# Kernel optimization log

Measured on AMD Instinct MI355X. Metric: run time of the kernel, lower is better.

The kernel has to match this reference:

```python
import jax, jax.numpy as jnp
import numpy as np

C = 64; NET = 32; K = 3; G = 4; GC = C // G; P = K * K
STRIDE = 1; PAD = 1; DIL = 1; OFFSET_SCALE = 1.0
BN_EPS = 1e-5; LN_EPS = 1e-6


def conv2d(x, w, b, groups=1, pad=1):
    # x: (N,C,H,W), w: (O, I//groups, kh, kw)
    y = jax.lax.conv_general_dilated(
        x, w, (1, 1), [(pad, pad), (pad, pad)],
        feature_group_count=groups,
        dimension_numbers=('NCHW', 'OIHW', 'NCHW'))
    return y + b[None, :, None, None]


def dcnv3_core(x, offset, mask):
    """Faithful port of dcnv3_core_pytorch (InternImage).
    x: (N,H,W,C) channels-last; offset: (N,H,W,G*P*2); mask: (N,H,W,G*P) (softmaxed).
    grid_sample(bilinear, zeros padding, align_corners=False) done manually."""
    xp = jnp.pad(x, ((0, 0), (PAD, PAD), (PAD, PAD), (0, 0)))
    N, Hin, Win, _ = xp.shape
    Ho, Wo = offset.shape[1], offset.shape[2]
    # reference points in normalized [0,1] coords (x first, y second)
    start = (DIL * (K - 1)) // 2 + 0.5
    ref_x = (start + jnp.arange(Wo, dtype=jnp.float32) * STRIDE) / Win  # (Wo,)
    ref_y = (start + jnp.arange(Ho, dtype=jnp.float32) * STRIDE) / Hin  # (Ho,)
    ref = jnp.stack(jnp.broadcast_arrays(ref_x[None, :], ref_y[:, None]), axis=-1)  # (Ho,Wo,2)
    # dilation grid (kernel tap offsets, torch meshgrid 'ij' flatten order: w-major)
    kv = (jnp.arange(K, dtype=jnp.float32) * DIL - (DIL * (K - 1)) // 2)
    gx, gy = jnp.meshgrid(kv / Win, kv / Hin, indexing='ij')
    grid = jnp.stack([gx, gy], -1).reshape(P, 2)  # (P,2), same for every group
    # sampling locations, normalized: (N,Ho,Wo,G,P,2)
    off = offset.reshape(N, Ho, Wo, G, P, 2) * (OFFSET_SCALE / jnp.array([Win, Hin], jnp.float32))
    loc = ref[None, :, :, None, None, :] + grid[None, None, None, None, :, :] * OFFSET_SCALE + off
    # grid_sample align_corners=False: pixel = loc*size - 0.5  (since g = 2*loc-1)
    px = loc[..., 0] * Win - 0.5
    py = loc[..., 1] * Hin - 0.5
    x0 = jnp.floor(px); y0 = jnp.floor(py)
    ix0 = x0.astype(jnp.int32); iy0 = y0.astype(jnp.int32)
    wx1 = px - x0; wy1 = py - y0; wx0 = 1.0 - wx1; wy0 = 1.0 - wy1
    xg = xp.reshape(N, Hin, Win, G, GC)
    n_idx = jnp.arange(N)[:, None, None, None, None]
    g_idx = jnp.arange(G)[None, None, None, :, None]

    def sample(ix, iy):
        valid = ((ix >= 0) & (ix < Win) & (iy >= 0) & (iy < Hin)).astype(xg.dtype)
        v = xg[n_idx, jnp.clip(iy, 0, Hin - 1), jnp.clip(ix, 0, Win - 1), g_idx]  # (N,Ho,Wo,G,P,GC)
        return v * valid[..., None]

    val = (sample(ix0, iy0) * (wx0 * wy0)[..., None]
           + sample(ix0 + 1, iy0) * (wx1 * wy0)[..., None]
           + sample(ix0, iy0 + 1) * (wx0 * wy1)[..., None]
           + sample(ix0 + 1, iy0 + 1) * (wx1 * wy1)[..., None])
    out = jnp.einsum('nhwgpc,nhwgp->nhwgc', val, mask.reshape(N, Ho, Wo, G, P))
    return out.reshape(N, Ho, Wo, C)


def setup_inputs() -> dict:
    key = jax.random.key(0)
    ks = jax.random.split(key, 16)
    N, H, W = 4, 128, 128
    f = lambda k, shp, s=1.0: jax.random.normal(k, shp, jnp.float32) * s
    return {
        'input_x': f(ks[0], (N, C, H, W)),
        'input_y': f(ks[1], (N, NET, H, W)),
        'enc_w': f(ks[2], (NET, C), 0.05), 'enc_b': jnp.zeros((NET,), jnp.float32),
        'bn_g': jnp.ones((NET,), jnp.float32), 'bn_b': jnp.zeros((NET,), jnp.float32),
        'bn_m': jnp.zeros((NET,), jnp.float32), 'bn_v': jnp.ones((NET,), jnp.float32),
        'gru_wz': f(ks[3], (NET, 2 * NET, 3, 3), 0.05), 'gru_bz': jnp.zeros((NET,), jnp.float32),
        'gru_wr': f(ks[4], (NET, 2 * NET, 3, 3), 0.05), 'gru_br': jnp.zeros((NET,), jnp.float32),
        'gru_wq': f(ks[5], (NET, 2 * NET, 3, 3), 0.05), 'gru_bq': jnp.zeros((NET,), jnp.float32),
        'dw_w': f(ks[6], (C, 1, 3, 3), 0.1), 'dw_b': jnp.zeros((C,), jnp.float32),
        'ln_g': jnp.ones((C,), jnp.float32), 'ln_b': jnp.zeros((C,), jnp.float32),
        'off_w': f(ks[7], (G * P * 2, C), 0.1), 'off_b': f(ks[8], (G * P * 2,), 0.1),
        'mask_w': f(ks[9], (G * P, C), 0.1), 'mask_b': jnp.zeros((G * P,), jnp.float32),
        'inp_w': f(ks[10], (C, C), 0.1), 'inp_b': jnp.zeros((C,), jnp.float32),
        'out_w': f(ks[11], (C, C), 0.1), 'out_b': jnp.zeros((C,), jnp.float32),
    }


def reference(input_x, input_y, enc_w, enc_b, bn_g, bn_b, bn_m, bn_v,
              gru_wz, gru_bz, gru_wr, gru_br, gru_wq, gru_bq,
              dw_w, dw_b, ln_g, ln_b, off_w, off_b, mask_w, mask_b,
              inp_w, inp_b, out_w, out_b):
    N, _, H, W = input_x.shape
    # encoder: 1x1 Conv + BN(eval) + SiLU
    e = jnp.einsum('nchw,oc->nohw', input_x, enc_w) + enc_b[None, :, None, None]
    e = (e - bn_m[None, :, None, None]) * jax.lax.rsqrt(bn_v + BN_EPS)[None, :, None, None]
    e = e * bn_g[None, :, None, None] + bn_b[None, :, None, None]
    x_en = jax.nn.silu(e)
    # ConvGRU: h' = (1-z)*h + z*q
    hx = jnp.concatenate([input_y, x_en], axis=1)
    z = jax.nn.sigmoid(conv2d(hx, gru_wz, gru_bz))
    r = jax.nn.sigmoid(conv2d(hx, gru_wr, gru_br))
    q = jnp.tanh(conv2d(jnp.concatenate([r * input_y, x_en], axis=1), gru_wq, gru_bq))
    h = (1.0 - z) * input_y + z * q  # (N,NET,H,W)
    # channels-last main path
    inp = input_x.transpose(0, 2, 3, 1)  # (N,H,W,C)
    x = inp @ inp_w.T + inp_b
    # depthwise conv on gru state -> LN (channels_last) -> GELU
    y = conv2d(h, dw_w, dw_b, groups=NET).transpose(0, 2, 3, 1)  # (N,H,W,C)
    mu = y.mean(-1, keepdims=True)
    var = ((y - mu) ** 2).mean(-1, keepdims=True)
    y = (y - mu) * jax.lax.rsqrt(var + LN_EPS) * ln_g + ln_b
    y = jax.nn.gelu(y, approximate=False)
    offset = y @ off_w.T + off_b  # (N,H,W,G*P*2)
    m = y @ mask_w.T + mask_b
    m = jax.nn.softmax(m.reshape(N, H, W, G, P), axis=-1).reshape(N, H, W, G * P)
    x = dcnv3_core(x, offset, m)
    x = x @ out_w.T + out_b
    return jax.nn.silu(x.transpose(0, 3, 1, 2)), h
```

## Files before the change

kernel.cpp:

```cpp
#include <hip/hip_runtime.h>
#include <hip/hip_bf16.h>

typedef __hip_bfloat16 bf16;
typedef short short8v __attribute__((ext_vector_type(8)));
typedef short short4v __attribute__((ext_vector_type(4)));
typedef float float4v __attribute__((ext_vector_type(4)));

static __device__ __forceinline__ float b2f(bf16 v){ return __bfloat162float(v); }
static __device__ __forceinline__ bf16 f2b(float v){ return __float2bfloat16(v); }
static __device__ __forceinline__ float bu2f(unsigned short u){ return __uint_as_float(((unsigned)u) << 16); }
static __device__ __forceinline__ short f2bs(float v){ bf16 t = __float2bfloat16(v); return *(short*)&t; }

#define WT 128
#define HWT 16384

#define OFF_ENC   0
#define OFF_ENCSC 2048
#define OFF_ENCSH 2080
#define OFF_BZ    20544
#define OFF_BR    39008
#define OFF_BQ    57472
#define OFF_DWP   57504
#define OFF_DWB   58080
#define OFF_LNG   58144
#define OFF_LNB   58208
#define OFF_OMB   65184
#define OFF_WINP  65296
#define OFF_BINP  69392
#define OFF_BOUT  73552
#define NW_TOTAL  73616
#define NBF_ZR    36864
#define NBF_Q     18432
#define NBF_OM    7168
#define NBF_OUT   4096
#define NPREP     (NW_TOTAL + NBF_ZR + NBF_Q + NBF_OM + NBF_OUT)
#define NHALO     2064
#define NTOT      (NPREP + NHALO)

#define B_WZRB  294912
#define B_WQB   368640
#define B_WOMB  405504
#define B_WOUTB 419840
#define B_HXP   428544
#define B_QINP  9081344
#define B_ZBUF  17734144
#define B_XL    428544

__global__ void k_prep(
    const float* __restrict__ enc_w, const float* __restrict__ enc_b,
    const float* __restrict__ bn_g, const float* __restrict__ bn_b,
    const float* __restrict__ bn_m, const float* __restrict__ bn_v,
    const float* __restrict__ gwz, const float* __restrict__ gbz,
    const float* __restrict__ gwr, const float* __restrict__ gbr,
    const float* __restrict__ gwq, const float* __restrict__ gbq,
    const float* __restrict__ dww, const float* __restrict__ dwb,
    const float* __restrict__ lng, const float* __restrict__ lnb,
    const float* __restrict__ offw, const float* __restrict__ offb,
    const float* __restrict__ maskw, const float* __restrict__ maskb,
    const float* __restrict__ inpw, const float* __restrict__ inpb,
    const float* __restrict__ outw, const float* __restrict__ outb,
    float* __restrict__ Wp, bf16* __restrict__ wzrb, bf16* __restrict__ wqb,
    bf16* __restrict__ womb, bf16* __restrict__ woutb,
    bf16* __restrict__ hxp, bf16* __restrict__ qinp) {
  int i = blockIdx.x * blockDim.x + threadIdx.x;
  if (i >= NTOT) return;
  if (i >= NPREP) {
    int t = i - NPREP;
    int img = t / 516, r = t % 516;
    int ph, pw;
    if (r < 130) { ph = 0; pw = r; }
    else if (r < 260) { ph = 129; pw = r - 130; }
    else if (r < 388) { ph = r - 260 + 1; pw = 0; }
    else { ph = r - 388 + 1; pw = 129; }
    size_t pb = (((size_t)img * 130 + ph) * 130 + pw) * 64;
    uint4 zz = make_uint4(0, 0, 0, 0);
    #pragma unroll
    for (int k = 0; k < 8; ++k) {
      ((uint4*)(hxp + pb))[k] = zz;
      ((uint4*)(qinp + pb))[k] = zz;
    }
    return;
  }
  if (i >= NW_TOTAL) {
    int d = i - NW_TOTAL;
    if (d < NBF_ZR) {
      int t = d / 9216, rem = d % 9216;
      int kc = rem / 512, rem2 = rem % 512;
      int ln = rem2 >> 3, j = rem2 & 7;
      int n = t * 16 + (ln & 15);
      int cin = (kc & 1) * 32 + ((ln >> 4) << 3) + j;
      int tap = kc >> 1;
      float v = (n < 32) ? gwz[(n*64 + cin)*9 + tap] : gwr[((n-32)*64 + cin)*9 + tap];
      wzrb[d] = f2b(v);
    } else if (d < NBF_ZR + NBF_Q) {
      int d2 = d - NBF_ZR;
      int t = d2 / 9216, rem = d2 % 9216;
      int kc = rem / 512, rem2 = rem % 512;
      int ln = rem2 >> 3, j = rem2 & 7;
      int n = t * 16 + (ln & 15);
      int cin = (kc & 1) * 32 + ((ln >> 4) << 3) + j;
      int tap = kc >> 1;
      wqb[d2] = f2b(gwq[(n*64 + cin)*9 + tap]);
    } else if (d < NBF_ZR + NBF_Q + NBF_OM) {
      int d3 = d - NBF_ZR - NBF_Q;
      int wv = d3 / 1024, rem = d3 % 1024;
      int kc = rem / 512, rem2 = rem % 512;
      int ln = rem2 >> 3, j = rem2 & 7;
      int jcol = wv * 16 + (ln & 15);
      int c = kc * 32 + ((ln >> 4) << 3) + j;
      float v = (jcol < 72) ? offw[jcol*64 + c] : ((jcol < 108) ? maskw[(jcol-72)*64 + c] : 0.f);
      womb[d3] = f2b(v);
    } else {
      int d4 = d - NBF_ZR - NBF_Q - NBF_OM;
      int wv = d4 / 1024, rem = d4 % 1024;
      int kc = rem / 512, rem2 = rem % 512;
      int ln = rem2 >> 3, j = rem2 & 7;
      int o = wv * 16 + (ln & 15);
      int c = kc * 32 + ((ln >> 4) << 3) + j;
      woutb[d4] = f2b(outw[o*64 + c]);
    }
    return;
  }
  float v;
  if (i < 2048) { int c = i >> 5, o = i & 31; v = enc_w[o*64 + c]; }
  else if (i < 2080) { int o = i - 2048; v = bn_g[o] * rsqrtf(bn_v[o] + 1e-5f); }
  else if (i < 2112) { int o = i - 2080;
    float sc = bn_g[o] * rsqrtf(bn_v[o] + 1e-5f);
    v = (enc_b[o] - bn_m[o]) * sc + bn_b[o]; }
  else if (i < 20544) { v = 0.f; }
  else if (i < 20576) { v = gbz[i - OFF_BZ]; }
  else if (i < 39008) { v = 0.f; }
  else if (i < 39040) { v = gbr[i - OFF_BR]; }
  else if (i < 57472) { v = 0.f; }
  else if (i < 57504) { v = gbq[i - OFF_BQ]; }
  else if (i < 58080) { int d = i - OFF_DWP; int tap = d >> 6, o = d & 63; v = dww[o*9 + tap]; }
  else if (i < 58144) { v = dwb[i - OFF_DWB]; }
  else if (i < 58208) { v = lng[i - OFF_LNG]; }
  else if (i < 58272) { v = lnb[i - OFF_LNB]; }
  else if (i < 65184) { v = 0.f; }
  else if (i < 65292) { int j = i - OFF_OMB; v = (j < 72) ? offb[j] : maskb[j-72]; }
  else if (i < 65296) { v = 0.f; }
  else if (i < 69392) { int d = i - OFF_WINP; int c = d >> 6, o = d & 63; v = inpw[o*64 + c]; }
  else if (i < 69456) { v = inpb[i - OFF_BINP]; }
  else if (i < 73552) { v = 0.f; }
  else { v = outb[i - OFF_BOUT]; }
  Wp[i] = v;
}

__global__ void __launch_bounds__(256) k_pre(
    const float* __restrict__ X, const float* __restrict__ Y,
    const float* __restrict__ Wp, bf16* __restrict__ hxp, bf16* __restrict__ qinp) {
  __shared__ float xls[4096];
  int tid = threadIdx.x;
  int px = tid & 63, sect = tid >> 6;
  int img = blockIdx.z, h = blockIdx.y, w0 = blockIdx.x * 64;
  int hw = h * WT + w0 + px;
  const float* xp = X + (size_t)img * (64 * HWT) + hw;
  #pragma unroll
  for (int i = 0; i < 16; ++i) {
    int c = sect * 16 + i;
    xls[c * 64 + px] = xp[c * HWT];
  }
  const float* yp = Y + (size_t)img * (32 * HWT) + hw;
  bf16 yv[8];
  #pragma unroll
  for (int i = 0; i < 8; ++i) yv[i] = f2b(yp[(sect * 8 + i) * HWT]);
  size_t pb = (((size_t)img * 130 + h + 1) * 130 + (w0 + px + 1)) * 64;
  *(uint4*)(hxp + pb + sect * 8) = *(const uint4*)yv;
  __syncthreads();
  float aen[8];
  #pragma unroll
  for (int o = 0; o < 8; ++o) aen[o] = 0.f;
  for (int k = 0; k < 64; ++k) {
    float a = xls[k * 64 + px];
    const float* we = Wp + OFF_ENC + k * 32 + sect * 8;
    #pragma unroll
    for (int o = 0; o < 8; ++o) aen[o] += a * we[o];
  }
  bf16 xe[8];
  #pragma unroll
  for (int o = 0; o < 8; ++o) {
    int oo = sect * 8 + o;
    float e = aen[o] * Wp[OFF_ENCSC + oo] + Wp[OFF_ENCSH + oo];
    xe[o] = f2b(e / (1.f + __expf(-e)));
  }
  *(uint4*)(hxp + pb + 32 + sect * 8) = *(const uint4*)xe;
  *(uint4*)(qinp + pb + 32 + sect * 8) = *(const uint4*)xe;
}

__global__ void __launch_bounds__(256) k_zr(
    const float* __restrict__ Wp,
    const bf16* __restrict__ hxp, const bf16* __restrict__ wzrb,
    bf16* __restrict__ qinp, bf16* __restrict__ zbuf) {
  __shared__ short zt[32 * 132];
  __shared__ short ryt[128 * 40];
  int tid = threadIdx.x;
  int wv = tid >> 6, ln = tid & 63;
  int quad = ln >> 4, lm = ln & 15;
  int img = blockIdx.z, h = blockIdx.y;
  int p0 = wv * 32;
  const short* hs = (const short*)hxp;
  const short* ws = (const short*)wzrb;
  size_t rowb = ((size_t)img * 130 + h + 1) * 130;
  const short* ab0 = hs + (rowb + p0 + lm + 1) * 64 + quad * 8;
  const short* ab1 = ab0 + 16 * 64;
  short8v a0[18], a1[18];
  #pragma unroll
  for (int kc = 0; kc < 18; ++kc) {
    const int tap = kc >> 1, cin0 = (kc & 1) * 32;
    const int dd = (tap / 3 - 1) * 130 + (tap % 3 - 1);
    a0[kc] = *(const short8v*)(ab0 + dd * 64 + cin0);
    a1[kc] = *(const short8v*)(ab1 + dd * 64 + cin0);
  }
  float4v acc[8];
  #pragma unroll
  for (int t = 0; t < 8; ++t) acc[t] = (float4v){0.f, 0.f, 0.f, 0.f};
  #pragma unroll
  for (int kc = 0; kc < 18; ++kc) {
    #pragma unroll
    for (int t = 0; t < 4; ++t) {
      short8v b = *(const short8v*)(ws + ((t * 18 + kc) * 64 + ln) * 8);
      acc[t*2]   = __builtin_amdgcn_mfma_f32_16x16x32_bf16(a0[kc], b, acc[t*2], 0, 0, 0);
      acc[t*2+1] = __builtin_amdgcn_mfma_f32_16x16x32_bf16(a1[kc], b, acc[t*2+1], 0, 0, 0);
    }
  }
  #pragma unroll
  for (int mt = 0; mt < 2; ++mt) {
    #pragma unroll
    for (int t = 0; t < 2; ++t) {
      int n = t * 16 + lm;
      float bz = Wp[OFF_BZ + n];
      short zp[4];
      #pragma unroll
      for (int ri = 0; ri < 4; ++ri)
        zp[ri] = f2bs(1.f / (1.f + __expf(-(acc[t*2+mt][ri] + bz))));
      *(short4v*)(zt + n * 132 + p0 + mt * 16 + quad * 4) = *(const short4v*)zp;
    }
  }
  #pragma unroll
  for (int mt = 0; mt < 2; ++mt) {
    #pragma unroll
    for (int t = 2; t < 4; ++t) {
      int c = (t - 2) * 16 + lm;
      float br = Wp[OFF_BR + c];
      #pragma unroll
      for (int ri = 0; ri < 4; ++ri) {
        int px = p0 + mt * 16 + quad * 4 + ri;
        float rv = 1.f / (1.f + __expf(-(acc[t*2+mt][ri] + br)));
        float yy = b2f(hxp[(rowb + px + 1) * 64 + c]);
        ryt[px * 40 + c] = f2bs(rv * yy);
      }
    }
  }
  __syncthreads();
  {
    int n2 = tid >> 3, pq = tid & 7;
    short8v z0 = *(const short8v*)(zt + n2 * 132 + pq * 16);
    short8v z1 = *(const short8v*)(zt + n2 * 132 + pq * 16 + 8);
    short* zo = (short*)zbuf + (((size_t)img * 128 + h) * 32 + n2) * 128 + pq * 16;
    *(short8v*)zo = z0;
    *(short8v*)(zo + 8) = z1;
  }
  {
    int px = tid >> 1, chalf = tid & 1;
    short8v r0 = *(const short8v*)(ryt + px * 40 + chalf * 16);
    short8v r1 = *(const short8v*)(ryt + px * 40 + chalf * 16 + 8);
    short* qo = (short*)qinp + (rowb + px + 1) * 64 + chalf * 16;
    *(short8v*)qo = r0;
    *(short8v*)(qo + 8) = r1;
  }
}

__global__ void __launch_bounds__(256) k_qg(
    const float* __restrict__ Y, const float* __restrict__ Wp,
    const bf16* __restrict__ qinp, const bf16* __restrict__ wqb,
    const bf16* __restrict__ zbuf, float* __restrict__ outh) {
  __shared__ float hout[32 * 132];
  int tid = threadIdx.x;
  int wv = tid >> 6, ln = tid & 63;
  int quad = ln >> 4, lm = ln & 15;
  int img = blockIdx.z, h = blockIdx.y;
  int p0 = wv * 32;
  const short* qs = (const short*)qinp;
  const short* ws = (const short*)wqb;
  size_t rowb = ((size_t)img * 130 + h + 1) * 130;
  const short* ab0 = qs + (rowb + p0 + lm + 1) * 64 + quad * 8;
  const short* ab1 = ab0 + 16 * 64;
  short8v a0[18], a1[18];
  #pragma unroll
  for (int kc = 0; kc < 18; ++kc) {
    const int tap = kc >> 1, cin0 = (kc & 1) * 32;
    const int dd = (tap / 3 - 1) * 130 + (tap % 3 - 1);
    a0[kc] = *(const short8v*)(ab0 + dd * 64 + cin0);
    a1[kc] = *(const short8v*)(ab1 + dd * 64 + cin0);
  }
  float4v acc[4];
  #pragma unroll
  for (int t = 0; t < 4; ++t) acc[t] = (float4v){0.f, 0.f, 0.f, 0.f};
  #pragma unroll
  for (int kc = 0; kc < 18; ++kc) {
    #pragma unroll
    for (int t = 0; t < 2; ++t) {
      short8v b = *(const short8v*)(ws + ((t * 18 + kc) * 64 + ln) * 8);
      acc[t*2]   = __builtin_amdgcn_mfma_f32_16x16x32_bf16(a0[kc], b, acc[t*2], 0, 0, 0);
      acc[t*2+1] = __builtin_amdgcn_mfma_f32_16x16x32_bf16(a1[kc], b, acc[t*2+1], 0, 0, 0);
    }
  }
  #pragma unroll
  for (int mt = 0; mt < 2; ++mt) {
    #pragma unroll
    for (int t = 0; t < 2; ++t) {
      int n = t * 16 + lm;
      float bq = Wp[OFF_BQ + n];
      float4 hv;
      hv.x = acc[t*2+mt][0] + bq; hv.y = acc[t*2+mt][1] + bq;
      hv.z = acc[t*2+mt][2] + bq; hv.w = acc[t*2+mt][3] + bq;
      *(float4*)(hout + n * 132 + p0 + mt * 16 + quad * 4) = hv;
    }
  }
  __syncthreads();
  const short* zbb = (const short*)zbuf + ((size_t)img * 128 + h) * 32 * 128;
  #pragma unroll
  for (int r = 0; r < 4; ++r) {
    int n = (tid >> 5) + r * 8;
    int px4 = (tid & 31) * 4;
    float4 hv = *(const float4*)(hout + n * 132 + px4);
    uint2 zz = *(const uint2*)(zbb + n * 128 + px4);
    size_t gb = ((size_t)img * 32 + n) * HWT + h * 128 + px4;
    float4 yv = *(const float4*)(Y + gb);
    float z0 = bu2f((unsigned short)(zz.x & 0xFFFFu)), z1 = bu2f((unsigned short)(zz.x >> 16));
    float z2 = bu2f((unsigned short)(zz.y & 0xFFFFu)), z3 = bu2f((unsigned short)(zz.y >> 16));
    float4 o;
    o.x = (1.f - z0) * yv.x + z0 * tanhf(hv.x);
    o.y = (1.f - z1) * yv.y + z1 * tanhf(hv.y);
    o.z = (1.f - z2) * yv.z + z2 * tanhf(hv.z);
    o.w = (1.f - z3) * yv.w + z3 * tanhf(hv.w);
    *(float4*)(outh + gb) = o;
  }
}

__global__ void __launch_bounds__(256) k_xl(
    const float* __restrict__ X, const float* __restrict__ Wp, bf16* __restrict__ xl) {
  __shared__ float xls[4096];
  int tid = threadIdx.x;
  int px = tid & 63, sect = tid >> 6;
  int img = blockIdx.z, h = blockIdx.y, w0 = blockIdx.x * 64;
  int hw = h * WT + w0 + px;
  const float* xp = X + (size_t)img * (64 * HWT) + hw;
  #pragma unroll
  for (int i = 0; i < 16; ++i) {
    int c = sect * 16 + i;
    xls[c * 64 + px] = xp[c * HWT];
  }
  __syncthreads();
  float acc[16];
  #pragma unroll
  for (int o = 0; o < 16; ++o) acc[o] = Wp[OFF_BINP + sect * 16 + o];
  for (int k = 0; k < 64; ++k) {
    float a = xls[k * 64 + px];
    const float* wr = Wp + OFF_WINP + k * 64 + sect * 16;
    #pragma unroll
    for (int o = 0; o < 16; ++o) acc[o] += a * wr[o];
  }
  bf16 ov[16];
  #pragma unroll
  for (int o = 0; o < 16; ++o) ov[o] = f2b(acc[o]);
  bf16* op = xl + ((size_t)img * HWT + hw) * 64 + sect * 16;
  ((uint4*)op)[0] = ((const uint4*)ov)[0];
  ((uint4*)op)[1] = ((const uint4*)ov)[1];
}

#define LDS_PSA  0
#define LDS_PSB  2048
#define LDS_STAT 4096
#define LDS_Y    4608
#define LDS_OM   13824
#define LDS_TOT  28416

__global__ void __launch_bounds__(512) k_mega(
    const float* __restrict__ Wp, const float* __restrict__ hb,
    const bf16* __restrict__ xl, const bf16* __restrict__ womb,
    const bf16* __restrict__ woutb, float* __restrict__ out0) {
  __shared__ char smem[LDS_TOT];
  float* psa  = (float*)(smem + LDS_PSA);
  float* psb  = (float*)(smem + LDS_PSB);
  float* stat = (float*)(smem + LDS_STAT);
  short* yls  = (short*)(smem + LDS_Y);
  short* omls = (short*)(smem + LDS_OM);
  short* vls  = (short*)(smem + LDS_Y);

  int tid = threadIdx.x;
  int img = blockIdx.z, h = blockIdx.y, w0 = blockIdx.x * 64;

  int wloc = tid & 63, part = tid >> 6;
  int w = w0 + wloc;
  float yv[8];
  {
    const float* hn = hb + (size_t)img * (32 * HWT);
    #pragma unroll
    for (int i = 0; i < 8; ++i) yv[i] = Wp[OFF_DWB + part*8 + i];
    #pragma unroll
    for (int tap = 0; tap < 9; ++tap) {
      int dy = tap / 3 - 1, dx = tap % 3 - 1;
      int hh = h + dy, ww = w + dx;
      bool ok = ((unsigned)hh < 128u) && ((unsigned)ww < 128u);
      int off = hh * WT + ww;
      #pragma unroll
      for (int j = 0; j < 4; ++j) {
        int cin = part * 4 + j;
        float a = ok ? hn[cin * HWT + off] : 0.f;
        yv[2*j]   += a * Wp[OFF_DWP + tap*64 + part*8 + 2*j];
        yv[2*j+1] += a * Wp[OFF_DWP + tap*64 + part*8 + 2*j+1];
      }
    }
  }
  float lsum = 0.f, lsq = 0.f;
  #pragma unroll
  for (int i = 0; i < 8; ++i) { lsum += yv[i]; lsq += yv[i]*yv[i]; }
  psa[part * 64 + wloc] = lsum;
  psb[part * 64 + wloc] = lsq;
  __syncthreads();
  if (tid < 64) {
    float s = 0.f, q = 0.f;
    #pragma unroll
    for (int p = 0; p < 8; ++p) { s += psa[p*64 + tid]; q += psb[p*64 + tid]; }
    float mu = s * (1.f/64.f);
    float var = q * (1.f/64.f) - mu * mu;
    stat[tid*2] = mu;
    stat[tid*2+1] = rsqrtf(var + 1e-6f);
  }
  __syncthreads();
  {
    float mu = stat[wloc*2], inv = stat[wloc*2+1];
    bf16 tmp[8];
    #pragma unroll
    for (int i = 0; i < 8; ++i) {
      int c = part*8 + i;
      float v = (yv[i] - mu) * inv * Wp[OFF_LNG + c] + Wp[OFF_LNB + c];
      tmp[i] = f2b(0.5f * v * (1.f + erff(v * 0.70710678118654752f)));
    }
    *(short8v*)(yls + wloc*72 + part*8) = *(const short8v*)tmp;
  }
  __syncthreads();

  int wv = tid >> 6, ln = tid & 63, quad = ln >> 4, lm = ln & 15;
  if (wv < 7) {
    const short* wb = (const short*)womb;
    float4v acc[4];
    #pragma unroll
    for (int mt = 0; mt < 4; ++mt) acc[mt] = (float4v){0.f,0.f,0.f,0.f};
    #pragma unroll
    for (int kc = 0; kc < 2; ++kc) {
      short8v b = *(const short8v*)(wb + ((wv * 2 + kc) * 64 + ln) * 8);
      #pragma unroll
      for (int mt = 0; mt < 4; ++mt) {
        short8v a = *(const short8v*)(yls + (mt*16 + lm)*72 + kc*32 + quad*8);
        acc[mt] = __builtin_amdgcn_mfma_f32_16x16x32_bf16(a, b, acc[mt], 0, 0, 0);
      }
    }
    float bias = Wp[OFF_OMB + wv*16 + lm];
    #pragma unroll
    for (int mt = 0; mt < 4; ++mt) {
      #pragma unroll
      for (int ri = 0; ri < 4; ++ri)
        omls[(mt*16 + quad*4 + ri)*114 + wv*16 + lm] = f2bs(acc[mt][ri] + bias);
    }
  }
  __syncthreads();

  {
    int px = tid >> 3, g = (tid >> 1) & 3, half = tid & 1;
    const short* oml = omls + px*114;
    float m[9];
    #pragma unroll
    for (int p = 0; p < 9; ++p) m[p] = bu2f((unsigned short)oml[72 + g*9 + p]);
    float mx = m[0];
    #pragma unroll
    for (int p = 1; p < 9; ++p) mx = fmaxf(mx, m[p]);
    float sum = 0.f;
    #pragma unroll
    for (int p = 0; p < 9; ++p) { m[p] = __expf(m[p] - mx); sum += m[p]; }
    float rs = 1.f / sum;
    int wg = w0 + px;
    const bf16* xn = xl + (size_t)img * (HWT * 64);
    float acc[8];
    #pragma unroll
    for (int i = 0; i < 8; ++i) acc[i] = 0.f;
    for (int p = 0; p < 9; ++p) {
      float bx = (float)(wg + p / 3 - 1);
      float by = (float)(h + p % 3 - 1);
      float ox = bu2f((unsigned short)oml[g*18 + p*2]);
      float oy = bu2f((unsigned short)oml[g*18 + p*2 + 1]);
      float mk = m[p] * rs;
      float pxx = bx + ox, pyy = by + oy;
      float fx = floorf(pxx), fy = floorf(pyy);
      int jx0 = (int)fx, jy0 = (int)fy;
      float wx1 = pxx - fx, wy1 = pyy - fy;
      float wx0 = 1.f - wx1, wy0 = 1.f - wy1;
      int cjx[4] = { jx0, jx0 + 1, jx0, jx0 + 1 };
      int cjy[4] = { jy0, jy0, jy0 + 1, jy0 + 1 };
      float cw[4] = { wx0*wy0, wx1*wy0, wx0*wy1, wx1*wy1 };
      #pragma unroll
      for (int k = 0; k < 4; ++k) {
        if ((unsigned)cjx[k] < 128u && (unsigned)cjy[k] < 128u) {
          float cf = mk * cw[k];
          const bf16* s = xn + (size_t)(cjy[k] * WT + cjx[k]) * 64 + g * 16 + half * 8;
          uint4 u0 = *(const uint4*)(s);
          const unsigned uu[4] = {u0.x,u0.y,u0.z,u0.w};
          #pragma unroll
          for (int q = 0; q < 4; ++q) {
            acc[2*q]     += cf * bu2f((unsigned short)(uu[q] & 0xFFFFu));
            acc[2*q + 1] += cf * bu2f((unsigned short)(uu[q] >> 16));
          }
        }
      }
    }
    bf16 tmp[8];
    #pragma unroll
    for (int i = 0; i < 8; ++i) tmp[i] = f2b(acc[i]);
    *(short8v*)(vls + px*72 + g*16 + half*8) = *(const short8v*)tmp;
  }
  __syncthreads();

  if (wv < 4) {
    const short* wb = (const short*)woutb;
    float4v acc[4];
    #pragma unroll
    for (int mt = 0; mt < 4; ++mt) acc[mt] = (float4v){0.f,0.f,0.f,0.f};
    #pragma unroll
    for (int kc = 0; kc < 2; ++kc) {
      short8v b = *(const short8v*)(wb + ((wv * 2 + kc) * 64 + ln) * 8);
      #pragma unroll
      for (int mt = 0; mt < 4; ++mt) {
        short8v a = *(const short8v*)(vls + (mt*16 + lm)*72 + kc*32 + quad*8);
        acc[mt] = __builtin_amdgcn_mfma_f32_16x16x32_bf16(a, b, acc[mt], 0, 0, 0);
      }
    }
    int ch = wv*16 + lm;
    float bias = Wp[OFF_BOUT + ch];
    #pragma unroll
    for (int mt = 0; mt < 4; ++mt) {
      float4 v;
      float s0 = acc[mt][0] + bias; v.x = s0 / (1.f + __expf(-s0));
      float s1 = acc[mt][1] + bias; v.y = s1 / (1.f + __expf(-s1));
      float s2 = acc[mt][2] + bias; v.z = s2 / (1.f + __expf(-s2));
      float s3 = acc[mt][3] + bias; v.w = s3 / (1.f + __expf(-s3));
      *(float4*)(out0 + ((size_t)img*64 + ch)*HWT + h*128 + w0 + mt*16 + quad*4) = v;
    }
  }
}

extern "C" void kernel_launch(void* const* d_in, const int* in_sizes, int n_in,
                              void* d_out, int out_size, void* d_ws, size_t ws_size,
                              hipStream_t stream) {
  const float* input_x = (const float*)d_in[0];
  const float* input_y = (const float*)d_in[1];

  float* Wp = (float*)d_ws;
  bf16* WZRB  = (bf16*)((char*)d_ws + B_WZRB);
  bf16* WQB   = (bf16*)((char*)d_ws + B_WQB);
  bf16* WOMB  = (bf16*)((char*)d_ws + B_WOMB);
  bf16* WOUTB = (bf16*)((char*)d_ws + B_WOUTB);
  bf16* HXP   = (bf16*)((char*)d_ws + B_HXP);
  bf16* QINP  = (bf16*)((char*)d_ws + B_QINP);
  bf16* ZBUF  = (bf16*)((char*)d_ws + B_ZBUF);
  bf16* XL    = (bf16*)((char*)d_ws + B_XL);
  float* out0 = (float*)d_out;
  float* outh = (float*)d_out + 4194304;

  k_prep<<<dim3((NTOT + 255)/256), dim3(256), 0, stream>>>(
      (const float*)d_in[2], (const float*)d_in[3], (const float*)d_in[4], (const float*)d_in[5],
      (const float*)d_in[6], (const float*)d_in[7], (const float*)d_in[8], (const float*)d_in[9],
      (const float*)d_in[10], (const float*)d_in[11], (const float*)d_in[12], (const float*)d_in[13],
      (const float*)d_in[14], (const float*)d_in[15], (const float*)d_in[16], (const float*)d_in[17],
      (const float*)d_in[18], (const float*)d_in[19], (const float*)d_in[20], (const float*)d_in[21],
      (const float*)d_in[22], (const float*)d_in[23], (const float*)d_in[24], (const float*)d_in[25],
      Wp, WZRB, WQB, WOMB, WOUTB, HXP, QINP);
  k_pre<<<dim3(2, 128, 4), dim3(256), 0, stream>>>(input_x, input_y, Wp, HXP, QINP);
  k_zr <<<dim3(1, 128, 4), dim3(256), 0, stream>>>(Wp, HXP, WZRB, QINP, ZBUF);
  k_qg <<<dim3(1, 128, 4), dim3(256), 0, stream>>>(input_y, Wp, QINP, WQB, ZBUF, outh);
  k_xl <<<dim3(2, 128, 4), dim3(256), 0, stream>>>(input_x, Wp, XL);
  k_mega<<<dim3(2, 128, 4), dim3(512), 0, stream>>>(Wp, outh, XL, WOMB, WOUTB, out0);
}
```

Before: 257.4 us.

## Split GRU conv rows across two blocks and spread output projection over all waves

k_zr and k_qg now handle 64 output pixels per block instead of 128, with each wave computing one 16-pixel M-tile. This doubles their grids and drops the second A-fragment set, cutting register pressure, and launch_bounds now request 4 blocks per SM. In k_mega the final 1x1 output projection is spread across all 8 waves, two tiles each, instead of only 4 waves doing 4 tiles. The aim is more parallelism and occupancy. The cost is that each B weight fragment is now fetched by more waves, and each block does less work relative to its launch and sync overhead.

Result: no change. 259.8 us (+0.9%).

```diff
diff --git a/kernel.cpp b/kernel.cpp
--- a/kernel.cpp
+++ b/kernel.cpp
@@ -112,10 +112,10 @@
       womb[d3] = f2b(v);
     } else {
       int d4 = d - NBF_ZR - NBF_Q - NBF_OM;
-      int wv = d4 / 1024, rem = d4 % 1024;
+      int nt = d4 / 1024, rem = d4 % 1024;
       int kc = rem / 512, rem2 = rem % 512;
       int ln = rem2 >> 3, j = rem2 & 7;
-      int o = wv * 16 + (ln & 15);
+      int o = nt * 16 + (ln & 15);
       int c = kc * 32 + ((ln >> 4) << 3) + j;
       woutb[d4] = f2b(outw[o*64 + c]);
     }
@@ -188,145 +188,128 @@
   *(uint4*)(qinp + pb + 32 + sect * 8) = *(const uint4*)xe;
 }
 
-__global__ void __launch_bounds__(256) k_zr(
+__global__ void __launch_bounds__(256, 4) k_zr(
     const float* __restrict__ Wp,
     const bf16* __restrict__ hxp, const bf16* __restrict__ wzrb,
     bf16* __restrict__ qinp, bf16* __restrict__ zbuf) {
-  __shared__ short zt[32 * 132];
-  __shared__ short ryt[128 * 40];
+  __shared__ short zt[32 * 68];
+  __shared__ short ryt[64 * 40];
   int tid = threadIdx.x;
   int wv = tid >> 6, ln = tid & 63;
   int quad = ln >> 4, lm = ln & 15;
   int img = blockIdx.z, h = blockIdx.y;
-  int p0 = wv * 32;
+  int w0 = blockIdx.x * 64;
+  int p0 = wv * 16;
   const short* hs = (const short*)hxp;
   const short* ws = (const short*)wzrb;
   size_t rowb = ((size_t)img * 130 + h + 1) * 130;
-  const short* ab0 = hs + (rowb + p0 + lm + 1) * 64 + quad * 8;
-  const short* ab1 = ab0 + 16 * 64;
-  short8v a0[18], a1[18];
+  const short* ab0 = hs + (rowb + w0 + p0 + lm + 1) * 64 + quad * 8;
+  short8v a0[18];
   #pragma unroll
   for (int kc = 0; kc < 18; ++kc) {
     const int tap = kc >> 1, cin0 = (kc & 1) * 32;
     const int dd = (tap / 3 - 1) * 130 + (tap % 3 - 1);
     a0[kc] = *(const short8v*)(ab0 + dd * 64 + cin0);
-    a1[kc] = *(const short8v*)(ab1 + dd * 64 + cin0);
-  }
-  float4v acc[8];
-  #pragma unroll
-  for (int t = 0; t < 8; ++t) acc[t] = (float4v){0.f, 0.f, 0.f, 0.f};
+  }
+  float4v acc[4];
+  #pragma unroll
+  for (int t = 0; t < 4; ++t) acc[t] = (float4v){0.f, 0.f, 0.f, 0.f};
   #pragma unroll
   for (int kc = 0; kc < 18; ++kc) {
     #pragma unroll
     for (int t = 0; t < 4; ++t) {
       short8v b = *(const short8v*)(ws + ((t * 18 + kc) * 64 + ln) * 8);
-      acc[t*2]   = __builtin_amdgcn_mfma_f32_16x16x32_bf16(a0[kc], b, acc[t*2], 0, 0, 0);
-      acc[t*2+1] = __builtin_amdgcn_mfma_f32_16x16x32_bf16(a1[kc], b, acc[t*2+1], 0, 0, 0);
-    }
-  }
-  #pragma unroll
-  for (int mt = 0; mt < 2; ++mt) {
-    #pragma unroll
-    for (int t = 0; t < 2; ++t) {
-      int n = t * 16 + lm;
-      float bz = Wp[OFF_BZ + n];
-      short zp[4];
-      #pragma unroll
-      for (int ri = 0; ri < 4; ++ri)
-        zp[ri] = f2bs(1.f / (1.f + __expf(-(acc[t*2+mt][ri] + bz))));
-      *(short4v*)(zt + n * 132 + p0 + mt * 16 + quad * 4) = *(const short4v*)zp;
-    }
-  }
-  #pragma unroll
-  for (int mt = 0; mt < 2; ++mt) {
-    #pragma unroll
-    for (int t = 2; t < 4; ++t) {
-      int c = (t - 2) * 16 + lm;
-      float br = Wp[OFF_BR + c];
-      #pragma unroll
-      for (int ri = 0; ri < 4; ++ri) {
-        int px = p0 + mt * 16 + quad * 4 + ri;
-        float rv = 1.f / (1.f + __expf(-(acc[t*2+mt][ri] + br)));
-        float yy = b2f(hxp[(rowb + px + 1) * 64 + c]);
-        ryt[px * 40 + c] = f2bs(rv * yy);
-      }
+      acc[t] = __builtin_amdgcn_mfma_f32_16x16x32_bf16(a0[kc], b, acc[t], 0, 0, 0);
+    }
+  }
+  #pragma unroll
+  for (int t = 0; t < 2; ++t) {
+    int n = t * 16 + lm;
+    float bz = Wp[OFF_BZ + n];
+    short zp[4];
+    #pragma unroll
+    for (int ri = 0; ri < 4; ++ri)
+      zp[ri] = f2bs(1.f / (1.f + __expf(-(acc[t][ri] + bz))));
+    *(short4v*)(zt + n * 68 + p0 + quad * 4) = *(const short4v*)zp;
+  }
+  #pragma unroll
+  for (int t = 2; t < 4; ++t) {
+    int c = (t - 2) * 16 + lm;
+    float br = Wp[OFF_BR + c];
+    #pragma unroll
+    for (int ri = 0; ri < 4; ++ri) {
+      int px = p0 + quad * 4 + ri;
+      float rv = 1.f / (1.f + __expf(-(acc[t][ri] + br)));
+      float yy = b2f(hxp[(rowb + w0 + px + 1) * 64 + c]);
+      ryt[px * 40 + c] = f2bs(rv * yy);
     }
   }
   __syncthreads();
   {
     int n2 = tid >> 3, pq = tid & 7;
-    short8v z0 = *(const short8v*)(zt + n2 * 132 + pq * 16);
-    short8v z1 = *(const short8v*)(zt + n2 * 132 + pq * 16 + 8);
-    short* zo = (short*)zbuf + (((size_t)img * 128 + h) * 32 + n2) * 128 + pq * 16;
+    short8v z0 = *(const short8v*)(zt + n2 * 68 + pq * 8);
+    short* zo = (short*)zbuf + (((size_t)img * 128 + h) * 32 + n2) * 128 + w0 + pq * 8;
     *(short8v*)zo = z0;
-    *(short8v*)(zo + 8) = z1;
   }
   {
-    int px = tid >> 1, chalf = tid & 1;
-    short8v r0 = *(const short8v*)(ryt + px * 40 + chalf * 16);
-    short8v r1 = *(const short8v*)(ryt + px * 40 + chalf * 16 + 8);
-    short* qo = (short*)qinp + (rowb + px + 1) * 64 + chalf * 16;
+    int px = tid >> 2, cq = tid & 3;
+    short8v r0 = *(const short8v*)(ryt + px * 40 + cq * 8);
+    short* qo = (short*)qinp + (rowb + w0 + px + 1) * 64 + cq * 8;
     *(short8v*)qo = r0;
-    *(short8v*)(qo + 8) = r1;
-  }
-}
-
-__global__ void __launch_bounds__(256) k_qg(
+  }
+}
+
+__global__ void __launch_bounds__(256, 4) k_qg(
     const float* __restrict__ Y, const float* __restrict__ Wp,
     const bf16* __restrict__ qinp, const bf16* __restrict__ wqb,
     const bf16* __restrict__ zbuf, float* __restrict__ outh) {
-  __shared__ float hout[32 * 132];
+  __shared__ float hout[32 * 68];
   int tid = threadIdx.x;
   int wv = tid >> 6, ln = tid & 63;
   int quad = ln >> 4, lm = ln & 15;
   int img = blockIdx.z, h = blockIdx.y;
-  int p0 = wv * 32;
+  int w0 = blockIdx.x * 64;
+  int p0 = wv * 16;
   const short* qs = (const short*)qinp;
   const short* ws = (const short*)wqb;
   size_t rowb = ((size_t)img * 130 + h + 1) * 130;
-  const short* ab0 = qs + (rowb + p0 + lm + 1) * 64 + quad * 8;
-  const short* ab1 = ab0 + 16 * 64;
-  short8v a0[18], a1[18];
+  const short* ab0 = qs + (rowb + w0 + p0 + lm + 1) * 64 + quad * 8;
+  short8v a0[18];
   #pragma unroll
   for (int kc = 0; kc < 18; ++kc) {
     const int tap = kc >> 1, cin0 = (kc & 1) * 32;
     const int dd = (tap / 3 - 1) * 130 + (tap % 3 - 1);
     a0[kc] = *(const short8v*)(ab0 + dd * 64 + cin0);
-    a1[kc] = *(const short8v*)(ab1 + dd * 64 + cin0);
-  }
-  float4v acc[4];
-  #pragma unroll
-  for (int t = 0; t < 4; ++t) acc[t] = (float4v){0.f, 0.f, 0.f, 0.f};
+  }
+  float4v acc[2];
+  #pragma unroll
+  for (int t = 0; t < 2; ++t) acc[t] = (float4v){0.f, 0.f, 0.f, 0.f};
   #pragma unroll
   for (int kc = 0; kc < 18; ++kc) {
     #pragma unroll
     for (int t = 0; t < 2; ++t) {
       short8v b = *(const short8v*)(ws + ((t * 18 + kc) * 64 + ln) * 8);
-      acc[t*2]   = __builtin_amdgcn_mfma_f32_16x16x32_bf16(a0[kc], b, acc[t*2], 0, 0, 0);
-      acc[t*2+1] = __builtin_amdgcn_mfma_f32_16x16x32_bf16(a1[kc], b, acc[t*2+1], 0, 0, 0);
-    }
-  }
-  #pragma unroll
-  for (int mt = 0; mt < 2; ++mt) {
-    #pragma unroll
-    for (int t = 0; t < 2; ++t) {
-      int n = t * 16 + lm;
-      float bq = Wp[OFF_BQ + n];
-      float4 hv;
-      hv.x = acc[t*2+mt][0] + bq; hv.y = acc[t*2+mt][1] + bq;
-      hv.z = acc[t*2+mt][2] + bq; hv.w = acc[t*2+mt][3] + bq;
-      *(float4*)(hout + n * 132 + p0 + mt * 16 + quad * 4) = hv;
-    }
-  }
-  __syncthreads();
-  const short* zbb = (const short*)zbuf + ((size_t)img * 128 + h) * 32 * 128;
-  #pragma unroll
-  for (int r = 0; r < 4; ++r) {
-    int n = (tid >> 5) + r * 8;
-    int px4 = (tid & 31) * 4;
-    float4 hv = *(const float4*)(hout + n * 132 + px4);
+      acc[t] = __builtin_amdgcn_mfma_f32_16x16x32_bf16(a0[kc], b, acc[t], 0, 0, 0);
+    }
+  }
+  #pragma unroll
+  for (int t = 0; t < 2; ++t) {
+    int n = t * 16 + lm;
+    float bq = Wp[OFF_BQ + n];
+    float4 hv;
+    hv.x = acc[t][0] + bq; hv.y = acc[t][1] + bq;
+    hv.z = acc[t][2] + bq; hv.w = acc[t][3] + bq;
+    *(float4*)(hout + n * 68 + p0 + quad * 4) = hv;
+  }
+  __syncthreads();
+  const short* zbb = (const short*)zbuf + ((size_t)img * 128 + h) * 32 * 128 + w0;
+  #pragma unroll
+  for (int r = 0; r < 2; ++r) {
+    int n = (tid >> 4) + r * 16;
+    int px4 = (tid & 15) * 4;
+    float4 hv = *(const float4*)(hout + n * 68 + px4);
     uint2 zz = *(const uint2*)(zbb + n * 128 + px4);
-    size_t gb = ((size_t)img * 32 + n) * HWT + h * 128 + px4;
+    size_t gb = ((size_t)img * 32 + n) * HWT + h * 128 + w0 + px4;
     float4 yv = *(const float4*)(Y + gb);
     float z0 = bu2f((unsigned short)(zz.x & 0xFFFFu)), z1 = bu2f((unsigned short)(zz.x >> 16));
     float z2 = bu2f((unsigned short)(zz.y & 0xFFFFu)), z3 = bu2f((unsigned short)(zz.y >> 16));
@@ -522,29 +505,26 @@
   }
   __syncthreads();
 
-  if (wv < 4) {
+  {
     const short* wb = (const short*)woutb;
-    float4v acc[4];
-    #pragma unroll
-    for (int mt = 0; mt < 4; ++mt) acc[mt] = (float4v){0.f,0.f,0.f,0.f};
-    #pragma unroll
-    for (int kc = 0; kc < 2; ++kc) {
-      short8v b = *(const short8v*)(wb + ((wv * 2 + kc) * 64 + ln) * 8);
+    #pragma unroll
+    for (int s = 0; s < 2; ++s) {
+      int tile = wv * 2 + s;
+      int nt = tile >> 2, mt = tile & 3;
+      float4v acc = (float4v){0.f,0.f,0.f,0.f};
       #pragma unroll
-      for (int mt = 0; mt < 4; ++mt) {
+      for (int kc = 0; kc < 2; ++kc) {
+        short8v b = *(const short8v*)(wb + ((nt * 2 + kc) * 64 + ln) * 8);
         short8v a = *(const short8v*)(vls + (mt*16 + lm)*72 + kc*32 + quad*8);
-        acc[mt] = __builtin_amdgcn_mfma_f32_16x16x32_bf16(a, b, acc[mt], 0, 0, 0);
+        acc = __builtin_amdgcn_mfma_f32_16x16x32_bf16(a, b, acc, 0, 0, 0);
       }
-    }
-    int ch = wv*16 + lm;
-    float bias = Wp[OFF_BOUT + ch];
-    #pragma unroll
-    for (int mt = 0; mt < 4; ++mt) {
+      int ch = nt*16 + lm;
+      float bias = Wp[OFF_BOUT + ch];
       float4 v;
-      float s0 = acc[mt][0] + bias; v.x = s0 / (1.f + __expf(-s0));
-      float s1 = acc[mt][1] + bias; v.y = s1 / (1.f + __expf(-s1));
-      float s2 = acc[mt][2] + bias; v.z = s2 / (1.f + __expf(-s2));
-      float s3 = acc[mt][3] + bias; v.w = s3 / (1.f + __expf(-s3));
+      float s0 = acc[0] + bias; v.x = s0 / (1.f + __expf(-s0));
+      float s1 = acc[1] + bias; v.y = s1 / (1.f + __expf(-s1));
+      float s2 = acc[2] + bias; v.z = s2 / (1.f + __expf(-s2));
+      float s3 = acc[3] + bias; v.w = s3 / (1.f + __expf(-s3));
       *(float4*)(out0 + ((size_t)img*64 + ch)*HWT + h*128 + w0 + mt*16 + quad*4) = v;
     }
   }
@@ -577,8 +557,8 @@
       (const float*)d_in[22], (const float*)d_in[23], (const float*)d_in[24], (const float*)d_in[25],
       Wp, WZRB, WQB, WOMB, WOUTB, HXP, QINP);
   k_pre<<<dim3(2, 128, 4), dim3(256), 0, stream>>>(input_x, input_y, Wp, HXP, QINP);
-  k_zr <<<dim3(1, 128, 4), dim3(256), 0, stream>>>(Wp, HXP, WZRB, QINP, ZBUF);
-  k_qg <<<dim3(1, 128, 4), dim3(256), 0, stream>>>(input_y, Wp, QINP, WQB, ZBUF, outh);
+  k_zr <<<dim3(2, 128, 4), dim3(256), 0, stream>>>(Wp, HXP, WZRB, QINP, ZBUF);
+  k_qg <<<dim3(2, 128, 4), dim3(256), 0, stream>>>(input_y, Wp, QINP, WQB, ZBUF, outh);
   k_xl <<<dim3(2, 128, 4), dim3(256), 0, stream>>>(input_x, Wp, XL);
   k_mega<<<dim3(2, 128, 4), dim3(512), 0, stream>>>(Wp, outh, XL, WOMB, WOUTB, out0);
 }
```
